# Kernel tuning notes

Hardware: AMD Instinct MI355X
Metric: run time of the kernel (lower is better)

Reference implementation:

```python
import jax, jax.numpy as jnp
import numpy as np

B = 16384
IN_DIM = 28 * 28
HID = 768
NUM_EXPERTS = 8
NUM_CLASSES = 10
H_PHASOR = 32          # phasor bank harmonics -> 2*H features
DELTA0 = 7.0
DECAY = 0.7            # spiking attention leak
THETA = 1.0
K_WINNERS = 5
TOP_K_ROUTE = 2
TRAITS = (0.6, 0.6, 0.5, 0.5, 0.4)


def setup_inputs() -> dict:
    key = jax.random.key(0)
    ks = jax.random.split(key, 16)
    s = 0.02
    return {
        "x": jax.random.normal(ks[0], (B, 28, 28), jnp.float32),
        "W_in": jax.random.normal(ks[1], (IN_DIM, HID), jnp.float32) * s,
        "b_in": jnp.zeros((HID,), jnp.float32),
        "W_ph": jax.random.normal(ks[2], (2 * H_PHASOR, HID), jnp.float32) * s,
        "b_ph": jnp.zeros((HID,), jnp.float32),
        "W_gate": jax.random.normal(ks[3], (HID, NUM_EXPERTS), jnp.float32) * s,
        "b_gate": jnp.zeros((NUM_EXPERTS,), jnp.float32),
        "W_exp": jax.random.normal(ks[4], (NUM_EXPERTS, HID, HID), jnp.float32) * s,
        "b_exp": jnp.zeros((NUM_EXPERTS, HID), jnp.float32),
        "W_th": jax.random.normal(ks[5], (HID, NUM_EXPERTS), jnp.float32) * s,
        "b_th": jnp.zeros((NUM_EXPERTS,), jnp.float32),
        "W_pm": jax.random.normal(ks[6], (5, NUM_EXPERTS), jnp.float32) * s,
        "b_pm": jnp.zeros((NUM_EXPERTS,), jnp.float32),
        "W_out": jax.random.normal(ks[7], (HID, NUM_CLASSES), jnp.float32) * s,
        "b_out": jnp.zeros((NUM_CLASSES,), jnp.float32),
    }


def reference(x, W_in, b_in, W_ph, b_ph, W_gate, b_gate, W_exp, b_exp,
              W_th, b_th, W_pm, b_pm, W_out, b_out):
    Bn = x.shape[0]
    x_flat = x.reshape((Bn, -1))
    proj = x_flat @ W_in + b_in                                  # [B, HID]

    # Phasor bank on per-sample mean activation: sin/cos at H harmonics
    x_mean = jnp.mean(proj, axis=-1)                             # [B]
    freqs = DELTA0 * jnp.arange(1, H_PHASOR + 1, dtype=proj.dtype)
    phase = x_mean[:, None] * freqs[None, :]                     # [B, H]
    feats = jnp.concatenate([jnp.sin(phase), jnp.cos(phase)], -1)  # [B, 2H]
    enhanced = proj + feats @ W_ph + b_ph                        # [B, HID]

    # Top-K index selection feeding gather/scatter spiking attention
    V = enhanced.shape[-1]
    K = min(32, V)
    topk_idx = jax.lax.top_k(enhanced, K)[1].astype(jnp.int32)   # [B, K]
    w = DECAY ** jnp.arange(K, dtype=enhanced.dtype)             # decaying drive

    def gains_fn(idx):
        v = jnp.zeros((V,), enhanced.dtype).at[idx].add(w)       # scatter-add
        vals, widx = jax.lax.top_k(v, K_WINNERS)                 # k-WTA
        return jnp.ones((V,), enhanced.dtype).at[widx].add(vals / THETA)

    gains = jax.vmap(gains_fn)(topk_idx)                         # [B, V]
    attended = enhanced * gains

    # Personality bias + thalamic bias (thalamic_scale = 1.0)
    traits = jnp.asarray(TRAITS, dtype=enhanced.dtype)
    pbias = traits @ W_pm + b_pm                                 # [E]
    thal = jnp.mean(attended, axis=0) @ W_th + b_th              # [E]

    # MoE retrieval core: gate -> top-k softmax route -> combine experts
    gate_logits = attended @ W_gate + b_gate + pbias[None] + thal[None]  # [B, E]
    gvals, gidx = jax.lax.top_k(gate_logits, TOP_K_ROUTE)        # [B, k]
    gw = jax.nn.softmax(gvals, axis=-1)                          # [B, k]
    exp_out = jnp.einsum('bh,ehd->bed', attended, W_exp) + b_exp[None]   # [B, E, HID]
    sel = jnp.take_along_axis(exp_out, gidx[:, :, None], axis=1)  # [B, k, HID]
    context = jnp.sum(gw[:, :, None] * sel, axis=1)              # [B, HID]

    return context @ W_out + b_out                               # [B, classes]
```

## Files before the change

kernel.cpp:

```cpp
#include <hip/hip_runtime.h>
#include <hip/hip_bf16.h>
#include <cstddef>

#define BATCH 16384
#define IND   784
#define HID   768
#define NEXP  8
#define KT13  13

typedef short bf16x8 __attribute__((ext_vector_type(8)));
typedef float f32x4  __attribute__((ext_vector_type(4)));
typedef unsigned short ushort_t;

#define GLD16(g, l)                                                            \
  __builtin_amdgcn_global_load_lds(                                            \
      (const __attribute__((address_space(1))) unsigned int*)(g),              \
      (__attribute__((address_space(3))) unsigned int*)(l), 16, 0, 0)

__global__ __launch_bounds__(256) void k_wtrans(const float* __restrict__ Wexp,
                                                __hip_bfloat16* __restrict__ Wt)
{
  __shared__ float tile[32][33];
  const int e = blockIdx.z;
  const int h0 = blockIdx.x * 32, d0 = blockIdx.y * 32;
  const int tx = threadIdx.x & 31, ty = threadIdx.x >> 5;
  const float* src = Wexp + ((size_t)e * HID + h0) * HID + d0;
  #pragma unroll
  for (int i = 0; i < 4; i++)
    tile[ty + 8 * i][tx] = src[(size_t)(ty + 8 * i) * HID + tx];
  __syncthreads();
  __hip_bfloat16* dst = Wt + ((size_t)e * HID + d0) * HID + h0;
  #pragma unroll
  for (int i = 0; i < 4; i++)
    dst[(size_t)(ty + 8 * i) * HID + tx] = __float2bfloat16(tile[tx][ty + 8 * i]);
}

__device__ inline ushort_t bf16_rne(float f) {
  union { float f; unsigned u; } v; v.f = f;
  unsigned r = v.u + 0x7fffu + ((v.u >> 16) & 1u);
  return (ushort_t)(r >> 16);
}
__device__ inline float bf16_to_f(ushort_t h) {
  union { unsigned u; float f; } v; v.u = ((unsigned)h) << 16;
  return v.f;
}

__global__ __launch_bounds__(256) void k_packA(const float* __restrict__ x,
                                               ushort_t* __restrict__ Ahi,
                                               ushort_t* __restrict__ Alo)
{
  const int kt = blockIdx.x, mt = blockIdx.y;
  const size_t tbase = ((size_t)mt * KT13 + kt) * 8192;
  const int kb = kt * 64;
  #pragma unroll
  for (int i = 0; i < 4; i++) {
    int id = i * 256 + threadIdx.x;
    int r = id >> 3, c = id & 7;
    int row = mt * 128 + r;
    int k0 = kb + c * 8;
    float v[8];
    if (k0 + 8 <= IND) {
      const float4* p = reinterpret_cast<const float4*>(x + (size_t)row * IND + k0);
      float4 a = p[0], b = p[1];
      v[0] = a.x; v[1] = a.y; v[2] = a.z; v[3] = a.w;
      v[4] = b.x; v[5] = b.y; v[6] = b.z; v[7] = b.w;
    } else {
      #pragma unroll
      for (int j = 0; j < 8; j++) v[j] = (k0 + j < IND) ? x[(size_t)row * IND + k0 + j] : 0.f;
    }
    ushort_t hi[8], lo[8];
    #pragma unroll
    for (int j = 0; j < 8; j++) {
      hi[j] = bf16_rne(v[j]);
      lo[j] = bf16_rne(v[j] - bf16_to_f(hi[j]));
    }
    size_t dst = tbase + (size_t)r * 64 + ((c ^ (r & 7)) * 8);
    *reinterpret_cast<uint4*>(Ahi + dst) = *reinterpret_cast<uint4*>(hi);
    *reinterpret_cast<uint4*>(Alo + dst) = *reinterpret_cast<uint4*>(lo);
  }
}

__global__ __launch_bounds__(256) void k_packB(const float* __restrict__ W,
                                               ushort_t* __restrict__ Bhi,
                                               ushort_t* __restrict__ Blo)
{
  const int kt = blockIdx.x, nt = blockIdx.y;
  const size_t tbase = ((size_t)nt * KT13 + kt) * 8192;
  const int kb = kt * 64;
  #pragma unroll
  for (int i = 0; i < 4; i++) {
    int id = i * 256 + threadIdx.x;
    int r = id >> 3, c = id & 7;
    int n = nt * 128 + r;
    int k0 = kb + c * 8;
    float v[8];
    #pragma unroll
    for (int j = 0; j < 8; j++)
      v[j] = (k0 + j < IND) ? W[(size_t)(k0 + j) * HID + n] : 0.f;
    ushort_t hi[8], lo[8];
    #pragma unroll
    for (int j = 0; j < 8; j++) {
      hi[j] = bf16_rne(v[j]);
      lo[j] = bf16_rne(v[j] - bf16_to_f(hi[j]));
    }
    size_t dst = tbase + (size_t)r * 64 + ((c ^ (r & 7)) * 8);
    *reinterpret_cast<uint4*>(Bhi + dst) = *reinterpret_cast<uint4*>(hi);
    *reinterpret_cast<uint4*>(Blo + dst) = *reinterpret_cast<uint4*>(lo);
  }
}

__global__ __launch_bounds__(256, 2) void k_proj2(const ushort_t* __restrict__ Ahi,
                                                  const ushort_t* __restrict__ Alo,
                                                  const ushort_t* __restrict__ Bhi,
                                                  const ushort_t* __restrict__ Blo,
                                                  const float* __restrict__ bias,
                                                  float* __restrict__ out)
{
  __shared__ __align__(16) ushort_t lds[4 * 8192];
  const int tid = threadIdx.x, lane = tid & 63, w = tid >> 6;
  const int mt = blockIdx.y, nt = blockIdx.x;
  const int m0 = (w >> 1) * 64, n0 = (w & 1) * 64;
  const int l15 = lane & 15, g = lane >> 4;

  f32x4 acc[4][4];
  #pragma unroll
  for (int i = 0; i < 4; i++)
    #pragma unroll
    for (int j = 0; j < 4; j++) acc[i][j] = (f32x4){0.f, 0.f, 0.f, 0.f};

  const size_t abase = (size_t)mt * KT13 * 8192;
  const size_t bbase = (size_t)nt * KT13 * 8192;

  for (int kt = 0; kt < KT13; kt++) {
    __syncthreads();
    const ushort_t* srcs[4] = { Ahi + abase + (size_t)kt * 8192,
                                Alo + abase + (size_t)kt * 8192,
                                Bhi + bbase + (size_t)kt * 8192,
                                Blo + bbase + (size_t)kt * 8192 };
    #pragma unroll
    for (int buf = 0; buf < 4; buf++) {
      #pragma unroll
      for (int i = 0; i < 4; i++) {
        int off = w * 2048 + i * 512 + lane * 8;
        GLD16(srcs[buf] + off, &lds[buf * 8192 + w * 2048 + i * 512]);
      }
    }
    asm volatile("s_waitcnt vmcnt(0)");
    __syncthreads();
    #pragma unroll
    for (int ks = 0; ks < 2; ks++) {
      bf16x8 ah[4], al[4], bh[4], bl[4];
      #pragma unroll
      for (int i = 0; i < 4; i++) {
        int ca = ((4 * ks + g) ^ (l15 & 7)) * 8;
        int ra = m0 + 16 * i + l15;
        ah[i] = *reinterpret_cast<const bf16x8*>(&lds[0 * 8192 + ra * 64 + ca]);
        al[i] = *reinterpret_cast<const bf16x8*>(&lds[1 * 8192 + ra * 64 + ca]);
        int rb = n0 + 16 * i + l15;
        bh[i] = *reinterpret_cast<const bf16x8*>(&lds[2 * 8192 + rb * 64 + ca]);
        bl[i] = *reinterpret_cast<const bf16x8*>(&lds[3 * 8192 + rb * 64 + ca]);
      }
      #pragma unroll
      for (int i = 0; i < 4; i++)
        #pragma unroll
        for (int j = 0; j < 4; j++) {
          acc[i][j] = __builtin_amdgcn_mfma_f32_16x16x32_bf16(ah[i], bh[j], acc[i][j], 0, 0, 0);
          acc[i][j] = __builtin_amdgcn_mfma_f32_16x16x32_bf16(ah[i], bl[j], acc[i][j], 0, 0, 0);
          acc[i][j] = __builtin_amdgcn_mfma_f32_16x16x32_bf16(al[i], bh[j], acc[i][j], 0, 0, 0);
        }
    }
  }
  #pragma unroll
  for (int i = 0; i < 4; i++) {
    #pragma unroll
    for (int q = 0; q < 4; q++) {
      int m = mt * 128 + m0 + 16 * i + g * 4 + q;
      #pragma unroll
      for (int j = 0; j < 4; j++) {
        int n = nt * 128 + n0 + 16 * j + l15;
        out[(size_t)m * HID + n] = acc[i][j][q] + bias[n];
      }
    }
  }
}

__global__ __launch_bounds__(256) void k_mean(const float* __restrict__ proj,
                                              float* __restrict__ means)
{
  const int t = threadIdx.x, lane = t & 63, w = t >> 6;
  const int row = blockIdx.x * 4 + w;
  const float* p = proj + (size_t)row * HID;
  float s = 0.f;
  #pragma unroll
  for (int j = 0; j < 12; j++) s += p[lane + 64 * j];
  #pragma unroll
  for (int off = 32; off; off >>= 1) s += __shfl_xor(s, off);
  if (lane == 0) means[row] = s * (1.0f / 768.0f);
}

__global__ __launch_bounds__(256) void k_phasor(const float* __restrict__ means,
                                                const float* __restrict__ Wph,
                                                const float* __restrict__ bph,
                                                float* __restrict__ enh)
{
  __shared__ float Fs[64][132];
  __shared__ float Ws[64][128];
  const int t  = threadIdx.x;
  const int bm = blockIdx.y * 128, bn = blockIdx.x * 128;
  {
    const int r = t >> 1;
    const float mn = means[bm + r];
    if ((t & 1) == 0) {
      #pragma unroll
      for (int j = 0; j < 32; j++) Fs[j][r] = sinf(mn * (7.0f * (j + 1)));
    } else {
      #pragma unroll
      for (int j = 0; j < 32; j++) Fs[32 + j][r] = cosf(mn * (7.0f * (j + 1)));
    }
  }
  #pragma unroll
  for (int i = 0; i < 8; i++) {
    int f4 = i * 256 + t;
    int k = f4 >> 5, n4 = (f4 & 31) * 4;
    *reinterpret_cast<float4*>(&Ws[k][n4]) =
        *reinterpret_cast<const float4*>(Wph + (size_t)k * HID + bn + n4);
  }
  __syncthreads();

  const int m0 = (t >> 4) * 8, n0 = (t & 15) * 8;
  float acc[8][8];
  #pragma unroll
  for (int i = 0; i < 8; i++)
    #pragma unroll
    for (int j = 0; j < 8; j++) acc[i][j] = 0.f;
  #pragma unroll 4
  for (int k = 0; k < 64; k++) {
    float a[8], b[8];
    *reinterpret_cast<float4*>(&a[0]) = *reinterpret_cast<const float4*>(&Fs[k][m0]);
    *reinterpret_cast<float4*>(&a[4]) = *reinterpret_cast<const float4*>(&Fs[k][m0 + 4]);
    *reinterpret_cast<float4*>(&b[0]) = *reinterpret_cast<const float4*>(&Ws[k][n0]);
    *reinterpret_cast<float4*>(&b[4]) = *reinterpret_cast<const float4*>(&Ws[k][n0 + 4]);
    #pragma unroll
    for (int i = 0; i < 8; i++)
      #pragma unroll
      for (int j = 0; j < 8; j++) acc[i][j] = fmaf(a[i], b[j], acc[i][j]);
  }
  float bl[8];
  #pragma unroll
  for (int j = 0; j < 8; j++) bl[j] = bph[bn + n0 + j];
  #pragma unroll
  for (int i = 0; i < 8; i++) {
    float* rowp = enh + (size_t)(bm + m0 + i) * HID + bn + n0;
    float4 p0 = *reinterpret_cast<float4*>(rowp);
    float4 p1 = *reinterpret_cast<float4*>(rowp + 4);
    p0.x += acc[i][0] + bl[0]; p0.y += acc[i][1] + bl[1];
    p0.z += acc[i][2] + bl[2]; p0.w += acc[i][3] + bl[3];
    p1.x += acc[i][4] + bl[4]; p1.y += acc[i][5] + bl[5];
    p1.z += acc[i][6] + bl[6]; p1.w += acc[i][7] + bl[7];
    *reinterpret_cast<float4*>(rowp)     = p0;
    *reinterpret_cast<float4*>(rowp + 4) = p1;
  }
}

__global__ __launch_bounds__(256) void k_attend(const float* __restrict__ enh,
                                                const float* __restrict__ Wg,
                                                __hip_bfloat16* __restrict__ attb,
                                                float* __restrict__ glog,
                                                float* __restrict__ partials)
{
  __shared__ float WgT[8][768];
  __shared__ float cs[4][768];
  const int t = threadIdx.x, lane = t & 63, w = t >> 6;
  for (int i = t; i < 768 * 8; i += 256) { int c = i >> 3, e = i & 7; WgT[e][c] = Wg[i]; }
  for (int i = t; i < 4 * 768; i += 256) cs[i / 768][i % 768] = 0.f;
  __syncthreads();

  for (int rr = 0; rr < 8; ++rr) {
    const int row = blockIdx.x * 32 + rr * 4 + w;
    const float* er = enh + (size_t)row * HID;
    float o[12], s[12];
    #pragma unroll
    for (int j = 0; j < 12; j++) { o[j] = er[lane + 64 * j]; s[j] = o[j]; }

    int wc[5];
    #pragma unroll
    for (int k = 0; k < 5; k++) {
      float v = -3.4e38f; int c = 0x7fffffff;
      #pragma unroll
      for (int j = 0; j < 12; j++)
        if (s[j] > v) { v = s[j]; c = lane + 64 * j; }
      #pragma unroll
      for (int off = 32; off; off >>= 1) {
        float ov = __shfl_xor(v, off); int oc = __shfl_xor(c, off);
        if (ov > v || (ov == v && oc < c)) { v = ov; c = oc; }
      }
      wc[k] = c;
      if (lane == (c & 63)) {
        #pragma unroll
        for (int j = 0; j < 12; j++) if (j == (c >> 6)) s[j] = -3.4e38f;
      }
    }

    float a[12];
    #pragma unroll
    for (int j = 0; j < 12; j++) a[j] = o[j];
    float wv = 1.0f;
    #pragma unroll
    for (int k = 0; k < 5; k++) {
      int c = wc[k];
      if (lane == (c & 63)) {
        #pragma unroll
        for (int j = 0; j < 12; j++) if (j == (c >> 6)) a[j] = o[j] * (1.0f + wv);
      }
      wv *= 0.7f;
    }
    #pragma unroll
    for (int j = 0; j < 12; j++)
      attb[(size_t)row * HID + lane + 64 * j] = __float2bfloat16(a[j]);
    #pragma unroll
    for (int j = 0; j < 12; j++) cs[w][lane + 64 * j] += a[j];

    float p[8];
    #pragma unroll
    for (int e = 0; e < 8; e++) p[e] = 0.f;
    #pragma unroll
    for (int j = 0; j < 12; j++) {
      int c = lane + 64 * j;
      #pragma unroll
      for (int e = 0; e < 8; e++) p[e] = fmaf(a[j], WgT[e][c], p[e]);
    }
    #pragma unroll
    for (int e = 0; e < 8; e++) {
      #pragma unroll
      for (int off = 32; off; off >>= 1) p[e] += __shfl_xor(p[e], off);
    }
    if (lane == 0) {
      #pragma unroll
      for (int e = 0; e < 8; e++) glog[(size_t)row * 8 + e] = p[e];
    }
  }
  __syncthreads();
  for (int i = t; i < 768; i += 256)
    partials[(size_t)blockIdx.x * 768 + i] = cs[0][i] + cs[1][i] + cs[2][i] + cs[3][i];
}

__global__ void k_thal(const float* __restrict__ partials,
                       const float* __restrict__ Wth, const float* __restrict__ bth,
                       const float* __restrict__ Wpm, const float* __restrict__ bpm,
                       const float* __restrict__ bgate, float* __restrict__ add8)
{
  __shared__ float cm[768];
  __shared__ float th[8];
  const int t = threadIdx.x;
  float s = 0.f;
  #pragma unroll 8
  for (int b = 0; b < 512; b++) s += partials[(size_t)b * 768 + t];
  cm[t] = s * (1.0f / 16384.0f);
  __syncthreads();
  if (t < 256) {
    int e = t >> 5, l = t & 31;
    float ps = 0.f;
    for (int c = l; c < 768; c += 32) ps = fmaf(cm[c], Wth[(size_t)c * 8 + e], ps);
    #pragma unroll
    for (int off = 16; off; off >>= 1) ps += __shfl_xor(ps, off);
    if (l == 0) th[e] = ps + bth[e];
  }
  __syncthreads();
  if (t < 8) {
    const float TR[5] = {0.6f, 0.6f, 0.5f, 0.5f, 0.4f};
    float pb = bpm[t];
    #pragma unroll
    for (int i = 0; i < 5; i++) pb = fmaf(TR[i], Wpm[i * 8 + t], pb);
    add8[t] = th[t] + pb + bgate[t];
  }
}

__global__ __launch_bounds__(256) void k_route(const float* __restrict__ glog,
                                               const float* __restrict__ add8,
                                               float* __restrict__ rw,
                                               unsigned char* __restrict__ re,
                                               int* __restrict__ counts)
{
  __shared__ float a8[8];
  __shared__ int lc[8];
  const int t = threadIdx.x;
  if (t < 8) { a8[t] = add8[t]; lc[t] = 0; }
  __syncthreads();
  const int row = blockIdx.x * 256 + t;
  const float4* gp = reinterpret_cast<const float4*>(glog + (size_t)row * 8);
  float4 g0 = gp[0], g1 = gp[1];
  float l[8] = { g0.x + a8[0], g0.y + a8[1], g0.z + a8[2], g0.w + a8[3],
                 g1.x + a8[4], g1.y + a8[5], g1.z + a8[6], g1.w + a8[7] };
  float v0 = l[0], v1 = -3.4e38f; int i0 = 0, i1 = 0;
  #pragma unroll
  for (int e = 1; e < 8; e++) {
    if (l[e] > v0)      { v1 = v0; i1 = i0; v0 = l[e]; i0 = e; }
    else if (l[e] > v1) { v1 = l[e]; i1 = e; }
  }
  float ex = expf(v1 - v0);
  float inv = 1.0f / (1.0f + ex);
  rw[row * 2] = inv; rw[row * 2 + 1] = ex * inv;
  re[row * 2] = (unsigned char)i0; re[row * 2 + 1] = (unsigned char)i1;
  atomicAdd(&lc[i0], 1); atomicAdd(&lc[i1], 1);
  __syncthreads();
  if (t < 8) atomicAdd(&counts[t], lc[t]);
}

__global__ void k_prefix(const int* __restrict__ counts, int* __restrict__ meta)
{
  if (threadIdx.x == 0) {
    int o = 0, tt = 0;
    for (int e = 0; e < 8; e++) {
      meta[e] = o; meta[9 + e] = tt; meta[19 + e] = o;
      o += counts[e]; tt += (counts[e] + 127) >> 7;
    }
    meta[8] = o; meta[17] = tt; meta[18] = tt;
  }
}

__global__ __launch_bounds__(256) void k_scatter(const unsigned char* __restrict__ re,
                                                 int* __restrict__ meta,
                                                 int* __restrict__ perm,
                                                 int* __restrict__ inv)
{
  __shared__ int lc[8], base[8];
  const int t = threadIdx.x;
  if (t < 8) lc[t] = 0;
  __syncthreads();
  const int row = blockIdx.x * 256 + t;
  const int e0 = re[row * 2], e1 = re[row * 2 + 1];
  const int p0 = atomicAdd(&lc[e0], 1);
  const int p1 = atomicAdd(&lc[e1], 1);
  __syncthreads();
  if (t < 8) base[t] = atomicAdd(&meta[19 + t], lc[t]);
  __syncthreads();
  const int s0 = base[e0] + p0;
  const int s1 = base[e1] + p1;
  perm[s0] = row * 2;     inv[row * 2]     = s0;
  perm[s1] = row * 2 + 1; inv[row * 2 + 1] = s1;
}

__global__ __launch_bounds__(256) void k_expert(const unsigned short* __restrict__ attb,
                                                const unsigned short* __restrict__ Wt,
                                                const float* __restrict__ bexp,
                                                const float* __restrict__ rw,
                                                const int* __restrict__ perm,
                                                const int* __restrict__ meta,
                                                ushort_t* __restrict__ ctxP)
{
  if ((int)blockIdx.x >= meta[18]) return;
  __shared__ __align__(16) unsigned short AsBs[2 * 128 * 64];
  __shared__ int rid[128];
  __shared__ float gws[128];
  __shared__ float bxs[128];
  unsigned short* As = AsBs;
  unsigned short* Bs = AsBs + 128 * 64;

  const int* tst = meta + 9;
  const int tb = blockIdx.x;
  int e = 0;
  #pragma unroll
  for (int i = 1; i < 8; i++) if (tb >= tst[i]) e = i;
  const int tix  = tb - tst[e];
  const int off  = meta[e];
  const int cnt  = meta[e + 1] - off;
  const int rbase = off + tix * 128;
  const int vcnt  = min(128, cnt - tix * 128);
  const int tid = threadIdx.x;
  const int nb  = blockIdx.y * 128;

  if (tid < 128) {
    if (tid < vcnt) {
      int p = perm[rbase + tid];
      rid[tid] = p >> 1; gws[tid] = rw[p];
    } else {
      rid[tid] = 0; gws[tid] = 0.f;
    }
    bxs[tid] = bexp[(size_t)e * HID + nb + tid];
  }
  __syncthreads();

  const int lane = tid & 63, w = tid >> 6;
  const int m0 = (w >> 1) * 64, n0 = (w & 1) * 64;
  const int l15 = lane & 15, g = lane >> 4;
  const unsigned short* wbase = Wt + ((size_t)e * HID + nb) * HID;

  f32x4 acc[4][4];
  #pragma unroll
  for (int i = 0; i < 4; i++)
    #pragma unroll
    for (int j = 0; j < 4; j++) acc[i][j] = (f32x4){0.f, 0.f, 0.f, 0.f};

  for (int kb = 0; kb < HID; kb += 64) {
    __syncthreads();
    #pragma unroll
    for (int i = 0; i < 4; i++) {
      int id = i * 256 + tid;
      int r = id >> 3, c = id & 7;
      int sc = (c ^ (r & 7)) * 8;
      GLD16(attb + (size_t)rid[r] * HID + kb + sc, As + (i * 256 + w * 64) * 8);
      GLD16(wbase + (size_t)r * HID + kb + sc,      Bs + (i * 256 + w * 64) * 8);
    }
    asm volatile("s_waitcnt vmcnt(0)");
    __syncthreads();
    #pragma unroll
    for (int ks = 0; ks < 2; ks++) {
      bf16x8 af[4], bfr[4];
      #pragma unroll
      for (int i = 0; i < 4; i++) {
        int ca = (((4 * ks + g) ^ (l15 & 7)) * 8);
        af[i]  = *reinterpret_cast<const bf16x8*>(As + (m0 + 16 * i + l15) * 64 + ca);
        bfr[i] = *reinterpret_cast<const bf16x8*>(Bs + (n0 + 16 * i + l15) * 64 + ca);
      }
      #pragma unroll
      for (int i = 0; i < 4; i++)
        #pragma unroll
        for (int j = 0; j < 4; j++)
          acc[i][j] = __builtin_amdgcn_mfma_f32_16x16x32_bf16(af[i], bfr[j], acc[i][j], 0, 0, 0);
    }
  }

  unsigned short* Cs = AsBs;
  __syncthreads();
  #pragma unroll
  for (int i = 0; i < 4; i++) {
    #pragma unroll
    for (int q = 0; q < 4; q++) {
      int m = m0 + 16 * i + g * 4 + q;
      float gwv = gws[m];
      #pragma unroll
      for (int j = 0; j < 4; j++) {
        int n = n0 + 16 * j + l15;
        Cs[m * 128 + n] = bf16_rne(gwv * (acc[i][j][q] + bxs[n]));
      }
    }
  }
  __syncthreads();
  #pragma unroll
  for (int c = 0; c < 8; c++) {
    int r = w * 32 + c * 4 + (lane >> 4);
    if (r < vcnt) {
      uint4 v = *reinterpret_cast<const uint4*>(Cs + r * 128 + l15 * 8);
      *reinterpret_cast<uint4*>(ctxP + (size_t)(rbase + r) * HID + nb + l15 * 8) = v;
    }
  }
}

__global__ __launch_bounds__(256) void k_out(const ushort_t* __restrict__ ctxP,
                                             const int* __restrict__ inv,
                                             const float* __restrict__ Wout,
                                             const float* __restrict__ bout,
                                             float* __restrict__ out)
{
  __shared__ float wT[10][768];
  const int t = threadIdx.x, lane = t & 63, w = t >> 6;
  for (int i = t; i < 7680; i += 256) { int cl = i / 768, d = i - cl * 768; wT[cl][d] = Wout[(size_t)d * 10 + cl]; }
  __syncthreads();
  for (int rr = 0; rr < 8; ++rr) {
    const int row = blockIdx.x * 32 + rr * 4 + w;
    const int s0 = inv[row * 2], s1 = inv[row * 2 + 1];
    const ushort_t* p0 = ctxP + (size_t)s0 * HID;
    const ushort_t* p1 = ctxP + (size_t)s1 * HID;
    float cd[12];
    #pragma unroll
    for (int j = 0; j < 12; j++)
      cd[j] = bf16_to_f(p0[lane + 64 * j]) + bf16_to_f(p1[lane + 64 * j]);
    float p[10];
    #pragma unroll
    for (int cl = 0; cl < 10; cl++) {
      float ps = 0.f;
      #pragma unroll
      for (int j = 0; j < 12; j++) ps = fmaf(cd[j], wT[cl][lane + 64 * j], ps);
      #pragma unroll
      for (int off = 32; off; off >>= 1) ps += __shfl_xor(ps, off);
      p[cl] = ps;
    }
    if (lane == 0) {
      #pragma unroll
      for (int cl = 0; cl < 10; cl++) out[(size_t)row * 10 + cl] = p[cl] + bout[cl];
    }
  }
}

extern "C" void kernel_launch(void* const* d_in, const int* in_sizes, int n_in,
                              void* d_out, int out_size, void* d_ws, size_t ws_size,
                              hipStream_t stream)
{
  const float* x     = (const float*)d_in[0];
  const float* W_in  = (const float*)d_in[1];
  const float* b_in  = (const float*)d_in[2];
  const float* W_ph  = (const float*)d_in[3];
  const float* b_ph  = (const float*)d_in[4];
  const float* W_g   = (const float*)d_in[5];
  const float* b_g   = (const float*)d_in[6];
  const float* W_exp = (const float*)d_in[7];
  const float* b_exp = (const float*)d_in[8];
  const float* W_th  = (const float*)d_in[9];
  const float* b_th  = (const float*)d_in[10];
  const float* W_pm  = (const float*)d_in[11];
  const float* b_pm  = (const float*)d_in[12];
  const float* W_out = (const float*)d_in[13];
  const float* b_out = (const float*)d_in[14];
  float* out = (float*)d_out;

  char* ws = (char*)d_ws;
  size_t off = 0;
  float* enh   = (float*)(ws + off); off += (size_t)BATCH * HID * 4;
  char*  aliasbase = ws + off;
  off += (size_t)BATCH * HID * 4;
  __hip_bfloat16* attb = (__hip_bfloat16*)(ws + off); off += (size_t)BATCH * HID * 2;
  __hip_bfloat16* Wt   = (__hip_bfloat16*)(ws + off); off += (size_t)NEXP * HID * HID * 2;
  float* glog     = (float*)(ws + off); off += (size_t)BATCH * 8 * 4;
  float* partials = (float*)(ws + off); off += (size_t)512 * 768 * 4;
  float* means    = (float*)(ws + off); off += (size_t)BATCH * 4;
  float* add8     = (float*)(ws + off); off += 256;
  float* rw       = (float*)(ws + off); off += (size_t)BATCH * 2 * 4;
  unsigned char* re = (unsigned char*)(ws + off); off += (size_t)BATCH * 2;
  int* counts = (int*)(ws + off); off += 256;
  int* meta   = (int*)(ws + off); off += 256;
  int* perm   = (int*)(ws + off); off += (size_t)BATCH * 2 * 4;
  int* invp   = (int*)(ws + off); off += (size_t)BATCH * 2 * 4;
  ushort_t* Bhi = (ushort_t*)(ws + off); off += (size_t)KT13 * 64 * HID * 2;
  ushort_t* Blo = (ushort_t*)(ws + off); off += (size_t)KT13 * 64 * HID * 2;
  ushort_t* Ahi = (ushort_t*)aliasbase;
  ushort_t* Alo = (ushort_t*)(aliasbase + (size_t)BATCH * KT13 * 64 * 2);
  ushort_t* ctxP = (ushort_t*)enh;

  hipMemsetAsync(counts, 0, 32, stream);
  k_wtrans<<<dim3(24, 24, 8), 256, 0, stream>>>(W_exp, Wt);
  k_packA <<<dim3(13, 128),   256, 0, stream>>>(x, Ahi, Alo);
  k_packB <<<dim3(13, 6),     256, 0, stream>>>(W_in, Bhi, Blo);
  k_proj2 <<<dim3(6, 128),    256, 0, stream>>>(Ahi, Alo, Bhi, Blo, b_in, enh);
  k_mean  <<<4096,            256, 0, stream>>>(enh, means);
  k_phasor<<<dim3(6, 128),    256, 0, stream>>>(means, W_ph, b_ph, enh);
  k_attend<<<512,             256, 0, stream>>>(enh, W_g, attb, glog, partials);
  k_thal  <<<1,               768, 0, stream>>>(partials, W_th, b_th, W_pm, b_pm, b_g, add8);
  k_route <<<64,              256, 0, stream>>>(glog, add8, rw, re, counts);
  k_prefix<<<1,                64, 0, stream>>>(counts, meta);
  k_scatter<<<64,             256, 0, stream>>>(re, meta, perm, invp);
  k_expert<<<dim3(264, 6),    256, 0, stream>>>((const unsigned short*)attb, (const unsigned short*)Wt,
                                                b_exp, rw, perm, meta, ctxP);
  k_out   <<<512,             256, 0, stream>>>(ctxP, invp, W_out, b_out, out);
}
```

Before: 340.8 us.

## Fuse x split-bf16 packing and row-mean into projection GEMM; double-buffer expert GEMM

The projection GEMM now reads fp32 x directly, converts it to hi/lo bf16 in registers and writes it into LDS, prefetching the next tile's x while the current one is converted. This removes the separate packA kernel and its round trip through memory. Per-row partial sums are produced in the epilogue so k_mean2 reduces 12 partials instead of re-reading the full projection. The expert GEMM gains double-buffered LDS staging, and its grid is reordered so the N tiles of one row block run next to each other. The cost is extra register pressure in the projection kernel and doubled LDS in the expert kernel, which may lower occupancy.

Result: no change. 342.8 us (+0.6%).

```diff
diff --git a/kernel.cpp b/kernel.cpp
--- a/kernel.cpp
+++ b/kernel.cpp
@@ -43,41 +43,6 @@
 __device__ inline float bf16_to_f(ushort_t h) {
   union { unsigned u; float f; } v; v.u = ((unsigned)h) << 16;
   return v.f;
-}
-
-__global__ __launch_bounds__(256) void k_packA(const float* __restrict__ x,
-                                               ushort_t* __restrict__ Ahi,
-                                               ushort_t* __restrict__ Alo)
-{
-  const int kt = blockIdx.x, mt = blockIdx.y;
-  const size_t tbase = ((size_t)mt * KT13 + kt) * 8192;
-  const int kb = kt * 64;
-  #pragma unroll
-  for (int i = 0; i < 4; i++) {
-    int id = i * 256 + threadIdx.x;
-    int r = id >> 3, c = id & 7;
-    int row = mt * 128 + r;
-    int k0 = kb + c * 8;
-    float v[8];
-    if (k0 + 8 <= IND) {
-      const float4* p = reinterpret_cast<const float4*>(x + (size_t)row * IND + k0);
-      float4 a = p[0], b = p[1];
-      v[0] = a.x; v[1] = a.y; v[2] = a.z; v[3] = a.w;
-      v[4] = b.x; v[5] = b.y; v[6] = b.z; v[7] = b.w;
-    } else {
-      #pragma unroll
-      for (int j = 0; j < 8; j++) v[j] = (k0 + j < IND) ? x[(size_t)row * IND + k0 + j] : 0.f;
-    }
-    ushort_t hi[8], lo[8];
-    #pragma unroll
-    for (int j = 0; j < 8; j++) {
-      hi[j] = bf16_rne(v[j]);
-      lo[j] = bf16_rne(v[j] - bf16_to_f(hi[j]));
-    }
-    size_t dst = tbase + (size_t)r * 64 + ((c ^ (r & 7)) * 8);
-    *reinterpret_cast<uint4*>(Ahi + dst) = *reinterpret_cast<uint4*>(hi);
-    *reinterpret_cast<uint4*>(Alo + dst) = *reinterpret_cast<uint4*>(lo);
-  }
 }
 
 __global__ __launch_bounds__(256) void k_packB(const float* __restrict__ W,
@@ -109,18 +74,20 @@
   }
 }
 
-__global__ __launch_bounds__(256, 2) void k_proj2(const ushort_t* __restrict__ Ahi,
-                                                  const ushort_t* __restrict__ Alo,
+__global__ __launch_bounds__(256, 2) void k_proj2(const float* __restrict__ x,
                                                   const ushort_t* __restrict__ Bhi,
                                                   const ushort_t* __restrict__ Blo,
                                                   const float* __restrict__ bias,
-                                                  float* __restrict__ out)
+                                                  float* __restrict__ out,
+                                                  float* __restrict__ pm)
 {
   __shared__ __align__(16) ushort_t lds[4 * 8192];
   const int tid = threadIdx.x, lane = tid & 63, w = tid >> 6;
   const int mt = blockIdx.y, nt = blockIdx.x;
   const int m0 = (w >> 1) * 64, n0 = (w & 1) * 64;
   const int l15 = lane & 15, g = lane >> 4;
+  const int ar = tid >> 1, ahf = tid & 1;
+  const float* xrow = x + (size_t)(mt * 128 + ar) * IND;
 
   f32x4 acc[4][4];
   #pragma unroll
@@ -128,48 +95,103 @@
     #pragma unroll
     for (int j = 0; j < 4; j++) acc[i][j] = (f32x4){0.f, 0.f, 0.f, 0.f};
 
-  const size_t abase = (size_t)mt * KT13 * 8192;
   const size_t bbase = (size_t)nt * KT13 * 8192;
 
-  for (int kt = 0; kt < KT13; kt++) {
-    __syncthreads();
-    const ushort_t* srcs[4] = { Ahi + abase + (size_t)kt * 8192,
-                                Alo + abase + (size_t)kt * 8192,
-                                Bhi + bbase + (size_t)kt * 8192,
-                                Blo + bbase + (size_t)kt * 8192 };
-    #pragma unroll
-    for (int buf = 0; buf < 4; buf++) {
-      #pragma unroll
-      for (int i = 0; i < 4; i++) {
-        int off = w * 2048 + i * 512 + lane * 8;
-        GLD16(srcs[buf] + off, &lds[buf * 8192 + w * 2048 + i * 512]);
-      }
-    }
-    asm volatile("s_waitcnt vmcnt(0)");
-    __syncthreads();
-    #pragma unroll
-    for (int ks = 0; ks < 2; ks++) {
-      bf16x8 ah[4], al[4], bh[4], bl[4];
-      #pragma unroll
-      for (int i = 0; i < 4; i++) {
-        int ca = ((4 * ks + g) ^ (l15 & 7)) * 8;
-        int ra = m0 + 16 * i + l15;
-        ah[i] = *reinterpret_cast<const bf16x8*>(&lds[0 * 8192 + ra * 64 + ca]);
-        al[i] = *reinterpret_cast<const bf16x8*>(&lds[1 * 8192 + ra * 64 + ca]);
-        int rb = n0 + 16 * i + l15;
-        bh[i] = *reinterpret_cast<const bf16x8*>(&lds[2 * 8192 + rb * 64 + ca]);
-        bl[i] = *reinterpret_cast<const bf16x8*>(&lds[3 * 8192 + rb * 64 + ca]);
-      }
-      #pragma unroll
-      for (int i = 0; i < 4; i++)
-        #pragma unroll
-        for (int j = 0; j < 4; j++) {
-          acc[i][j] = __builtin_amdgcn_mfma_f32_16x16x32_bf16(ah[i], bh[j], acc[i][j], 0, 0, 0);
-          acc[i][j] = __builtin_amdgcn_mfma_f32_16x16x32_bf16(ah[i], bl[j], acc[i][j], 0, 0, 0);
-          acc[i][j] = __builtin_amdgcn_mfma_f32_16x16x32_bf16(al[i], bh[j], acc[i][j], 0, 0, 0);
-        }
-    }
-  }
+#define XLOAD(kt, X)                                                           \
+  { int kb_ = (kt) * 64;                                                       \
+    _Pragma("unroll")                                                          \
+    for (int cc = 0; cc < 4; cc++) {                                           \
+      int c_ = ahf * 4 + cc;                                                   \
+      int k0_ = kb_ + c_ * 8;                                                  \
+      const float4* p_ = reinterpret_cast<const float4*>(xrow + (k0_ < IND ? k0_ : 0)); \
+      X[2 * cc]     = p_[0];                                                   \
+      X[2 * cc + 1] = p_[1];                                                   \
+    } }
+
+#define CVTW(kt, X)                                                            \
+  { int kb_ = (kt) * 64;                                                       \
+    _Pragma("unroll")                                                          \
+    for (int cc = 0; cc < 4; cc++) {                                           \
+      int c_ = ahf * 4 + cc;                                                   \
+      bool v_ = (kb_ + c_ * 8) < IND;                                          \
+      float f_[8];                                                             \
+      *reinterpret_cast<float4*>(&f_[0]) = X[2 * cc];                          \
+      *reinterpret_cast<float4*>(&f_[4]) = X[2 * cc + 1];                      \
+      ushort_t hi_[8], lo_[8];                                                 \
+      _Pragma("unroll")                                                        \
+      for (int j = 0; j < 8; j++) {                                            \
+        float fv_ = v_ ? f_[j] : 0.f;                                          \
+        hi_[j] = bf16_rne(fv_);                                                \
+        lo_[j] = bf16_rne(fv_ - bf16_to_f(hi_[j]));                            \
+      }                                                                        \
+      int dst_ = ar * 64 + ((c_ ^ (ar & 7)) * 8);                              \
+      *reinterpret_cast<uint4*>(&lds[0 * 8192 + dst_]) = *reinterpret_cast<uint4*>(hi_); \
+      *reinterpret_cast<uint4*>(&lds[1 * 8192 + dst_]) = *reinterpret_cast<uint4*>(lo_); \
+    } }
+
+#define GLDB(kt)                                                               \
+  { const ushort_t* bh_ = Bhi + bbase + (size_t)(kt) * 8192;                   \
+    const ushort_t* bl_ = Blo + bbase + (size_t)(kt) * 8192;                   \
+    _Pragma("unroll")                                                          \
+    for (int i = 0; i < 4; i++) {                                              \
+      int off_ = w * 2048 + i * 512 + lane * 8;                                \
+      GLD16(bh_ + off_, &lds[2 * 8192 + w * 2048 + i * 512]);                  \
+      GLD16(bl_ + off_, &lds[3 * 8192 + w * 2048 + i * 512]);                  \
+    } }
+
+#define MFMAPH()                                                               \
+  { _Pragma("unroll")                                                          \
+    for (int ks = 0; ks < 2; ks++) {                                           \
+      bf16x8 fah[4], fal[4], fbh[4], fbl[4];                                   \
+      _Pragma("unroll")                                                        \
+      for (int i = 0; i < 4; i++) {                                            \
+        int ca_ = ((4 * ks + g) ^ (l15 & 7)) * 8;                              \
+        int ra_ = m0 + 16 * i + l15;                                           \
+        fah[i] = *reinterpret_cast<const bf16x8*>(&lds[0 * 8192 + ra_ * 64 + ca_]); \
+        fal[i] = *reinterpret_cast<const bf16x8*>(&lds[1 * 8192 + ra_ * 64 + ca_]); \
+        int rb_ = n0 + 16 * i + l15;                                           \
+        fbh[i] = *reinterpret_cast<const bf16x8*>(&lds[2 * 8192 + rb_ * 64 + ca_]); \
+        fbl[i] = *reinterpret_cast<const bf16x8*>(&lds[3 * 8192 + rb_ * 64 + ca_]); \
+      }                                                                        \
+      _Pragma("unroll")                                                        \
+      for (int i = 0; i < 4; i++)                                              \
+        _Pragma("unroll")                                                      \
+        for (int j = 0; j < 4; j++) {                                          \
+          acc[i][j] = __builtin_amdgcn_mfma_f32_16x16x32_bf16(fah[i], fbh[j], acc[i][j], 0, 0, 0); \
+          acc[i][j] = __builtin_amdgcn_mfma_f32_16x16x32_bf16(fah[i], fbl[j], acc[i][j], 0, 0, 0); \
+          acc[i][j] = __builtin_amdgcn_mfma_f32_16x16x32_bf16(fal[i], fbh[j], acc[i][j], 0, 0, 0); \
+        }                                                                      \
+    } }
+
+#define PITER(kt, XC, XN, LAST)                                                \
+  GLDB(kt);                                                                    \
+  asm volatile("s_waitcnt vmcnt(8)" ::: "memory");                             \
+  if (!(LAST)) { XLOAD((kt) + 1, XN); }                                        \
+  CVTW(kt, XC);                                                                \
+  if (LAST) { asm volatile("s_waitcnt vmcnt(0)" ::: "memory"); }               \
+  else      { asm volatile("s_waitcnt vmcnt(8)" ::: "memory"); }               \
+  asm volatile("s_waitcnt lgkmcnt(0)" ::: "memory");                           \
+  __builtin_amdgcn_s_barrier();                                                \
+  MFMAPH();                                                                    \
+  __builtin_amdgcn_s_barrier();
+
+  float4 xa[8], xb[8];
+  XLOAD(0, xa);
+  for (int kt2 = 0; kt2 < 12; kt2 += 2) {
+    PITER(kt2,     xa, xb, 0);
+    PITER(kt2 + 1, xb, xa, 0);
+  }
+  PITER(12, xa, xb, 1);
+
+#undef XLOAD
+#undef CVTW
+#undef GLDB
+#undef MFMAPH
+#undef PITER
+
+  float bl[8];
+  #pragma unroll
+  for (int j = 0; j < 4; j++) bl[j] = bias[nt * 128 + n0 + 16 * j + l15];
   #pragma unroll
   for (int i = 0; i < 4; i++) {
     #pragma unroll
@@ -178,24 +200,33 @@
       #pragma unroll
       for (int j = 0; j < 4; j++) {
         int n = nt * 128 + n0 + 16 * j + l15;
-        out[(size_t)m * HID + n] = acc[i][j][q] + bias[n];
+        out[(size_t)m * HID + n] = acc[i][j][q] + bl[j];
       }
     }
   }
-}
-
-__global__ __launch_bounds__(256) void k_mean(const float* __restrict__ proj,
-                                              float* __restrict__ means)
-{
-  const int t = threadIdx.x, lane = t & 63, w = t >> 6;
-  const int row = blockIdx.x * 4 + w;
-  const float* p = proj + (size_t)row * HID;
+  const float blsum = bl[0] + bl[1] + bl[2] + bl[3];
+  const size_t pslot = (size_t)(nt * 2 + (w & 1)) * BATCH;
+  #pragma unroll
+  for (int i = 0; i < 4; i++) {
+    #pragma unroll
+    for (int q = 0; q < 4; q++) {
+      float s = acc[i][0][q] + acc[i][1][q] + acc[i][2][q] + acc[i][3][q] + blsum;
+      s += __shfl_xor(s, 1); s += __shfl_xor(s, 2);
+      s += __shfl_xor(s, 4); s += __shfl_xor(s, 8);
+      if (l15 == 0)
+        pm[pslot + mt * 128 + m0 + 16 * i + g * 4 + q] = s;
+    }
+  }
+}
+
+__global__ __launch_bounds__(256) void k_mean2(const float* __restrict__ pm,
+                                               float* __restrict__ means)
+{
+  const int row = blockIdx.x * 256 + threadIdx.x;
   float s = 0.f;
   #pragma unroll
-  for (int j = 0; j < 12; j++) s += p[lane + 64 * j];
-  #pragma unroll
-  for (int off = 32; off; off >>= 1) s += __shfl_xor(s, off);
-  if (lane == 0) means[row] = s * (1.0f / 768.0f);
+  for (int k = 0; k < 12; k++) s += pm[(size_t)k * BATCH + row];
+  means[row] = s * (1.0f / 768.0f);
 }
 
 __global__ __launch_bounds__(256) void k_phasor(const float* __restrict__ means,
@@ -448,16 +479,14 @@
                                                 const int* __restrict__ meta,
                                                 ushort_t* __restrict__ ctxP)
 {
-  if ((int)blockIdx.x >= meta[18]) return;
-  __shared__ __align__(16) unsigned short AsBs[2 * 128 * 64];
+  if ((int)blockIdx.y >= meta[18]) return;
+  __shared__ __align__(16) ushort_t sst[2][2][8192];
   __shared__ int rid[128];
   __shared__ float gws[128];
   __shared__ float bxs[128];
-  unsigned short* As = AsBs;
-  unsigned short* Bs = AsBs + 128 * 64;
 
   const int* tst = meta + 9;
-  const int tb = blockIdx.x;
+  const int tb = blockIdx.y;
   int e = 0;
   #pragma unroll
   for (int i = 1; i < 8; i++) if (tb >= tst[i]) e = i;
@@ -467,7 +496,7 @@
   const int rbase = off + tix * 128;
   const int vcnt  = min(128, cnt - tix * 128);
   const int tid = threadIdx.x;
-  const int nb  = blockIdx.y * 128;
+  const int nb  = blockIdx.x * 128;
 
   if (tid < 128) {
     if (tid < vcnt) {
@@ -485,24 +514,33 @@
   const int l15 = lane & 15, g = lane >> 4;
   const unsigned short* wbase = Wt + ((size_t)e * HID + nb) * HID;
 
+#define ESTAGE(kb, b)                                                          \
+  { _Pragma("unroll")                                                          \
+    for (int i = 0; i < 4; i++) {                                              \
+      int id_ = i * 256 + tid; int r_ = id_ >> 3, c_ = id_ & 7;                \
+      int sc_ = (c_ ^ (r_ & 7)) * 8;                                           \
+      GLD16(attb + (size_t)rid[r_] * HID + (kb) + sc_, &sst[b][0][(i * 256 + w * 64) * 8]); \
+      GLD16(wbase + (size_t)r_ * HID + (kb) + sc_,     &sst[b][1][(i * 256 + w * 64) * 8]); \
+    } }
+
   f32x4 acc[4][4];
   #pragma unroll
   for (int i = 0; i < 4; i++)
     #pragma unroll
     for (int j = 0; j < 4; j++) acc[i][j] = (f32x4){0.f, 0.f, 0.f, 0.f};
 
-  for (int kb = 0; kb < HID; kb += 64) {
-    __syncthreads();
-    #pragma unroll
-    for (int i = 0; i < 4; i++) {
-      int id = i * 256 + tid;
-      int r = id >> 3, c = id & 7;
-      int sc = (c ^ (r & 7)) * 8;
-      GLD16(attb + (size_t)rid[r] * HID + kb + sc, As + (i * 256 + w * 64) * 8);
-      GLD16(wbase + (size_t)r * HID + kb + sc,      Bs + (i * 256 + w * 64) * 8);
-    }
-    asm volatile("s_waitcnt vmcnt(0)");
-    __syncthreads();
+  ESTAGE(0, 0);
+  for (int t = 0; t < 12; t++) {
+    const int cb = t & 1;
+    if (t < 11) {
+      ESTAGE((t + 1) * 64, cb ^ 1);
+      asm volatile("s_waitcnt vmcnt(8)" ::: "memory");
+    } else {
+      asm volatile("s_waitcnt vmcnt(0)" ::: "memory");
+    }
+    __builtin_amdgcn_s_barrier();
+    const ushort_t* As = &sst[cb][0][0];
+    const ushort_t* Bs = &sst[cb][1][0];
     #pragma unroll
     for (int ks = 0; ks < 2; ks++) {
       bf16x8 af[4], bfr[4];
@@ -518,9 +556,11 @@
         for (int j = 0; j < 4; j++)
           acc[i][j] = __builtin_amdgcn_mfma_f32_16x16x32_bf16(af[i], bfr[j], acc[i][j], 0, 0, 0);
     }
-  }
-
-  unsigned short* Cs = AsBs;
+    __builtin_amdgcn_s_barrier();
+  }
+#undef ESTAGE
+
+  unsigned short* Cs = &sst[0][0][0];
   __syncthreads();
   #pragma unroll
   for (int i = 0; i < 4; i++) {
@@ -606,12 +646,11 @@
   char* ws = (char*)d_ws;
   size_t off = 0;
   float* enh   = (float*)(ws + off); off += (size_t)BATCH * HID * 4;
-  char*  aliasbase = ws + off;
-  off += (size_t)BATCH * HID * 4;
   __hip_bfloat16* attb = (__hip_bfloat16*)(ws + off); off += (size_t)BATCH * HID * 2;
   __hip_bfloat16* Wt   = (__hip_bfloat16*)(ws + off); off += (size_t)NEXP * HID * HID * 2;
   float* glog     = (float*)(ws + off); off += (size_t)BATCH * 8 * 4;
   float* partials = (float*)(ws + off); off += (size_t)512 * 768 * 4;
+  float* pm       = (float*)(ws + off); off += (size_t)12 * BATCH * 4;
   float* means    = (float*)(ws + off); off += (size_t)BATCH * 4;
   float* add8     = (float*)(ws + off); off += 256;
   float* rw       = (float*)(ws + off); off += (size_t)BATCH * 2 * 4;
@@ -622,23 +661,20 @@
   int* invp   = (int*)(ws + off); off += (size_t)BATCH * 2 * 4;
   ushort_t* Bhi = (ushort_t*)(ws + off); off += (size_t)KT13 * 64 * HID * 2;
   ushort_t* Blo = (ushort_t*)(ws + off); off += (size_t)KT13 * 64 * HID * 2;
-  ushort_t* Ahi = (ushort_t*)aliasbase;
-  ushort_t* Alo = (ushort_t*)(aliasbase + (size_t)BATCH * KT13 * 64 * 2);
   ushort_t* ctxP = (ushort_t*)enh;
 
   hipMemsetAsync(counts, 0, 32, stream);
   k_wtrans<<<dim3(24, 24, 8), 256, 0, stream>>>(W_exp, Wt);
-  k_packA <<<dim3(13, 128),   256, 0, stream>>>(x, Ahi, Alo);
   k_packB <<<dim3(13, 6),     256, 0, stream>>>(W_in, Bhi, Blo);
-  k_proj2 <<<dim3(6, 128),    256, 0, stream>>>(Ahi, Alo, Bhi, Blo, b_in, enh);
-  k_mean  <<<4096,            256, 0, stream>>>(enh, means);
+  k_proj2 <<<dim3(6, 128),    256, 0, stream>>>(x, Bhi, Blo, b_in, enh, pm);
+  k_mean2 <<<64,              256, 0, stream>>>(pm, means);
   k_phasor<<<dim3(6, 128),    256, 0, stream>>>(means, W_ph, b_ph, enh);
   k_attend<<<512,             256, 0, stream>>>(enh, W_g, attb, glog, partials);
   k_thal  <<<1,               768, 0, stream>>>(partials, W_th, b_th, W_pm, b_pm, b_g, add8);
   k_route <<<64,              256, 0, stream>>>(glog, add8, rw, re, counts);
   k_prefix<<<1,                64, 0, stream>>>(counts, meta);
   k_scatter<<<64,             256, 0, stream>>>(re, meta, perm, invp);
-  k_expert<<<dim3(264, 6),    256, 0, stream>>>((const unsigned short*)attb, (const unsigned short*)Wt,
+  k_expert<<<dim3(6, 264),    256, 0, stream>>>((const unsigned short*)attb, (const unsigned short*)Wt,
                                                 b_exp, rw, perm, meta, ctxP);
   k_out   <<<512,             256, 0, stream>>>(ctxP, invp, W_out, b_out, out);
 }
```
